# Optimization experiments

Hardware: AMD Instinct MI355X
Metric: run time of the kernel (lower is better)

Reference implementation:

```python
import jax, jax.numpy as jnp
import numpy as np

B, N, IN_DIM, HID = 8, 4096, 256, 256


def setup_inputs() -> dict:
    key = jax.random.key(0)
    ks = jax.random.split(key, 7)
    s_in = 1.0 / np.sqrt(IN_DIM)
    return {
        "x": jax.random.normal(ks[0], (B, N, IN_DIM), dtype=jnp.float32),
        "Wq": jax.random.uniform(ks[1], (IN_DIM, HID), jnp.float32, -s_in, s_in),
        "bq": jax.random.uniform(ks[2], (HID,), jnp.float32, -s_in, s_in),
        "Wk": jax.random.uniform(ks[3], (IN_DIM, HID), jnp.float32, -s_in, s_in),
        "bk": jax.random.uniform(ks[4], (HID,), jnp.float32, -s_in, s_in),
        "Wv": jax.random.uniform(ks[5], (IN_DIM, HID), jnp.float32, -s_in, s_in),
        "bv": jax.random.uniform(ks[6], (HID,), jnp.float32, -s_in, s_in),
    }


def reference(x, Wq, bq, Wk, bk, Wv, bv):
    # x: [B, N, in_dim]
    Q = jnp.einsum("bnd,dh->bnh", x, Wq) + bq  # [B, N, H]
    K = jnp.einsum("bnd,dh->bnh", x, Wk) + bk
    V = jnp.einsum("bnd,dh->bnh", x, Wv) + bv
    scale = 1.0 / jnp.sqrt(jnp.asarray(K.shape[-1], dtype=x.dtype))
    scores = jnp.einsum("bqh,bkh->bqk", Q, K) * scale  # [B, N, N]
    attn = jax.nn.softmax(scores, axis=-1)
    out = jnp.einsum("bqk,bkh->bqh", attn, V)  # [B, N, H]
    return out.mean(axis=1)  # [B, H]
```

## Files before the change

### kernel.cpp

```cpp
#include <hip/hip_runtime.h>
#include <hip/hip_bf16.h>


#define NTOK 4096
#define HDIM 256
#define NBATCH 8
#define SCALE 0.0625f

typedef __attribute__((ext_vector_type(8))) short short8_t;
typedef __attribute__((ext_vector_type(16))) float f32x16;

__device__ __forceinline__ unsigned short f2bf(float f) {
    unsigned u = __float_as_uint(f);
    u += 0x7fff + ((u >> 16) & 1);
    return (unsigned short)(u >> 16);
}

#define MFMA(a, b, c) __builtin_amdgcn_mfma_f32_32x32x16_bf16(a, b, c, 0, 0, 0)

__device__ __forceinline__ void async_cp16(const void* g, void* l) {
    __builtin_amdgcn_global_load_lds((const __attribute__((address_space(1))) void*)g,
                                     (__attribute__((address_space(3))) void*)l, 16, 0, 0);
}

__device__ __forceinline__ void stage_swz(unsigned short* lds, const unsigned short* src,
                                          int row0, int dbase, int w, int l) {
#pragma unroll
    for (int i = 0; i < 4; ++i) {
        int rloc = w * 32 + i * 8 + (l >> 3);
        int u = (l & 7) ^ (l >> 3);
        const unsigned short* g = src + (size_t)(row0 + rloc) * HDIM + dbase + u * 8;
        unsigned short* d = lds + (w * 32 + i * 8) * 64;
        async_cp16(g, d);
    }
}

__device__ __forceinline__ short8_t frd(const unsigned short* lds, int rb, int lo, int u) {
    return *(const short8_t*)(lds + ((rb * 32 + lo) * 8 + (u ^ (lo & 7))) * 8);
}

__global__ void zero_kernel(float* __restrict__ w, float* __restrict__ l, float* __restrict__ out) {
    int i = blockIdx.x * 256 + threadIdx.x;
    w[i] = 0.f;
    l[i] = 0.f;
    if (i < NBATCH * HDIM) out[i] = 0.f;
}

__global__ void convert_x(const float* __restrict__ x, unsigned short* __restrict__ xbf) {
    int i = (blockIdx.x * 256 + threadIdx.x) * 4;
    float4 v = *(const float4*)(x + i);
    ushort4 o;
    o.x = f2bf(v.x); o.y = f2bf(v.y); o.z = f2bf(v.z); o.w = f2bf(v.w);
    *(ushort4*)(xbf + i) = o;
}

__global__ void convert_wt(const float* __restrict__ Wq, const float* __restrict__ Wk,
                           const float* __restrict__ Wv, unsigned short* __restrict__ Wt) {
    int z = blockIdx.y;
    const float* W = (z == 0) ? Wq : (z == 1) ? Wk : Wv;
    unsigned short* o = Wt + z * 65536;
    int n = threadIdx.x;
    for (int kk = 0; kk < 32; ++kk) {
        int k = blockIdx.x * 32 + kk;
        o[n * 256 + k] = f2bf(W[k * 256 + n]);
    }
}

__global__ __launch_bounds__(256) void qkv_mfma(const unsigned short* __restrict__ xbf,
                                                const unsigned short* __restrict__ Wt,
                                                const float* __restrict__ bq, const float* __restrict__ bk,
                                                const float* __restrict__ bv,
                                                unsigned short* __restrict__ Qbf,
                                                unsigned short* __restrict__ Kbf,
                                                float* __restrict__ Vf) {
    const int z = blockIdx.z;
    const unsigned short* Wz = Wt + z * 65536;
    const float* bias = (z == 0) ? bq : (z == 1) ? bk : bv;
    const int m0 = blockIdx.x * 128, n0 = blockIdx.y * 128;
    const int t = threadIdx.x, w = t >> 6, l = t & 63, lo = l & 31, hi = l >> 5;
    const int rm = (w & 1) * 2, rn = (w >> 1) * 2;

    __shared__ __align__(16) char smem[32768];
    unsigned short* Xb = (unsigned short*)smem;
    unsigned short* Wb = (unsigned short*)(smem + 16384);

    f32x16 acc[2][2];
#pragma unroll
    for (int a = 0; a < 2; ++a)
#pragma unroll
        for (int c = 0; c < 2; ++c)
#pragma unroll
            for (int r = 0; r < 16; ++r) acc[a][c][r] = 0.f;

    for (int dc = 0; dc < 4; ++dc) {
        __syncthreads();
        stage_swz(Xb, xbf, m0, dc * 64, w, l);
        stage_swz(Wb, Wz, n0, dc * 64, w, l);
        __syncthreads();
#pragma unroll
        for (int ks = 0; ks < 4; ++ks) {
            int u = ks * 2 + hi;
            short8_t a0 = frd(Xb, rm + 0, lo, u);
            short8_t a1 = frd(Xb, rm + 1, lo, u);
            short8_t b0 = frd(Wb, rn + 0, lo, u);
            short8_t b1 = frd(Wb, rn + 1, lo, u);
            acc[0][0] = MFMA(a0, b0, acc[0][0]);
            acc[0][1] = MFMA(a0, b1, acc[0][1]);
            acc[1][0] = MFMA(a1, b0, acc[1][0]);
            acc[1][1] = MFMA(a1, b1, acc[1][1]);
        }
    }
    float bc0 = bias[n0 + (w >> 1) * 64 + lo];
    float bc1 = bias[n0 + (w >> 1) * 64 + 32 + lo];
#pragma unroll
    for (int mb = 0; mb < 2; ++mb)
#pragma unroll
        for (int r = 0; r < 16; ++r) {
            int row = m0 + (w & 1) * 64 + mb * 32 + (r & 3) + 8 * (r >> 2) + 4 * hi;
            int c0 = n0 + (w >> 1) * 64 + lo, c1 = c0 + 32;
            float v0 = acc[mb][0][r] + bc0;
            float v1 = acc[mb][1][r] + bc1;
            if (z == 2) {
                Vf[(size_t)row * HDIM + c0] = v0;
                Vf[(size_t)row * HDIM + c1] = v1;
            } else {
                unsigned short* o = (z == 0) ? Qbf : Kbf;
                o[(size_t)row * HDIM + c0] = f2bf(v0);
                o[(size_t)row * HDIM + c1] = f2bf(v1);
            }
        }
}

__global__ __launch_bounds__(256) void score_pass1(const unsigned short* __restrict__ Qbf,
                                                   const unsigned short* __restrict__ Kbf,
                                                   float* __restrict__ lsum) {
    const int b = blockIdx.z;
    const int q0 = blockIdx.x * 128;
    const int kslice = blockIdx.y;
    const int t = threadIdx.x, w = t >> 6, l = t & 63, lo = l & 31, hi = l >> 5;
    const int rq = (w & 1) * 2, rk = (w >> 1) * 2;
    const unsigned short* Qb = Qbf + (size_t)b * NTOK * HDIM;
    const unsigned short* Kb = Kbf + (size_t)b * NTOK * HDIM;

    __shared__ __align__(16) char smem[33792];
    unsigned short* Qs = (unsigned short*)smem;
    unsigned short* Ks = Qs + 8192;
    float* red = (float*)smem;

    float rs[2][16];
#pragma unroll
    for (int mb = 0; mb < 2; ++mb)
#pragma unroll
        for (int r = 0; r < 16; ++r) rs[mb][r] = 0.f;

    for (int kt = 0; kt < 4; ++kt) {
        const int k0 = kslice * 512 + kt * 128;
        f32x16 acc[2][2];
#pragma unroll
        for (int a = 0; a < 2; ++a)
#pragma unroll
            for (int c = 0; c < 2; ++c)
#pragma unroll
                for (int r = 0; r < 16; ++r) acc[a][c][r] = 0.f;

        for (int dc = 0; dc < 4; ++dc) {
            __syncthreads();
            stage_swz(Qs, Qb, q0, dc * 64, w, l);
            stage_swz(Ks, Kb, k0, dc * 64, w, l);
            __syncthreads();
#pragma unroll
            for (int ks = 0; ks < 4; ++ks) {
                int u = ks * 2 + hi;
                short8_t a0 = frd(Qs, rq + 0, lo, u);
                short8_t a1 = frd(Qs, rq + 1, lo, u);
                short8_t b0 = frd(Ks, rk + 0, lo, u);
                short8_t b1 = frd(Ks, rk + 1, lo, u);
                acc[0][0] = MFMA(a0, b0, acc[0][0]);
                acc[0][1] = MFMA(a0, b1, acc[0][1]);
                acc[1][0] = MFMA(a1, b0, acc[1][0]);
                acc[1][1] = MFMA(a1, b1, acc[1][1]);
            }
        }
#pragma unroll
        for (int mb = 0; mb < 2; ++mb)
#pragma unroll
            for (int r = 0; r < 16; ++r)
                rs[mb][r] += __expf(acc[mb][0][r] * SCALE) + __expf(acc[mb][1][r] * SCALE);
    }
    __syncthreads();
#pragma unroll
    for (int mb = 0; mb < 2; ++mb)
#pragma unroll
        for (int r = 0; r < 16; ++r) {
            int row = (w & 1) * 64 + mb * 32 + (r & 3) + 8 * (r >> 2) + 4 * hi;
            red[row * 66 + (w >> 1) * 32 + lo] = rs[mb][r];
        }
    __syncthreads();
    if (t < 128) {
        float s = 0.f;
#pragma unroll 8
        for (int j = 0; j < 64; ++j) s += red[t * 66 + j];
        atomicAdd(&lsum[b * NTOK + q0 + t], s);
    }
}

__global__ __launch_bounds__(256) void score_pass2(const unsigned short* __restrict__ Qbf,
                                                   const unsigned short* __restrict__ Kbf,
                                                   const float* __restrict__ lsum,
                                                   float* __restrict__ wsum) {
    const int b = blockIdx.z;
    const int k0 = blockIdx.x * 128;
    const int qslice = blockIdx.y;
    const int t = threadIdx.x, w = t >> 6, l = t & 63, lo = l & 31, hi = l >> 5;
    const int rq = (w & 1) * 2, rk = (w >> 1) * 2;
    const unsigned short* Qb = Qbf + (size_t)b * NTOK * HDIM;
    const unsigned short* Kb = Kbf + (size_t)b * NTOK * HDIM;

    __shared__ __align__(16) char smem[33792];
    __shared__ float linv_s[128];
    unsigned short* Qs = (unsigned short*)smem;
    unsigned short* Ks = Qs + 8192;
    float* red2 = (float*)smem;

    float cs0 = 0.f, cs1 = 0.f;

    for (int qt = 0; qt < 4; ++qt) {
        const int q0 = qslice * 512 + qt * 128;
        f32x16 acc[2][2];
#pragma unroll
        for (int a = 0; a < 2; ++a)
#pragma unroll
            for (int c = 0; c < 2; ++c)
#pragma unroll
                for (int r = 0; r < 16; ++r) acc[a][c][r] = 0.f;

        for (int dc = 0; dc < 4; ++dc) {
            __syncthreads();
            stage_swz(Qs, Qb, q0, dc * 64, w, l);
            stage_swz(Ks, Kb, k0, dc * 64, w, l);
            if (dc == 0 && t < 128) linv_s[t] = 1.0f / lsum[b * NTOK + q0 + t];
            __syncthreads();
#pragma unroll
            for (int ks = 0; ks < 4; ++ks) {
                int u = ks * 2 + hi;
                short8_t a0 = frd(Qs, rq + 0, lo, u);
                short8_t a1 = frd(Qs, rq + 1, lo, u);
                short8_t b0 = frd(Ks, rk + 0, lo, u);
                short8_t b1 = frd(Ks, rk + 1, lo, u);
                acc[0][0] = MFMA(a0, b0, acc[0][0]);
                acc[0][1] = MFMA(a0, b1, acc[0][1]);
                acc[1][0] = MFMA(a1, b0, acc[1][0]);
                acc[1][1] = MFMA(a1, b1, acc[1][1]);
            }
        }
#pragma unroll
        for (int mb = 0; mb < 2; ++mb)
#pragma unroll
            for (int r = 0; r < 16; ++r) {
                float li = linv_s[(w & 1) * 64 + mb * 32 + (r & 3) + 8 * (r >> 2) + 4 * hi];
                cs0 += __expf(acc[mb][0][r] * SCALE) * li;
                cs1 += __expf(acc[mb][1][r] * SCALE) * li;
            }
    }
    __syncthreads();
    red2[((w >> 1) * 64 + lo) * 5 + (w & 1) * 2 + hi] = cs0;
    red2[((w >> 1) * 64 + 32 + lo) * 5 + (w & 1) * 2 + hi] = cs1;
    __syncthreads();
    if (t < 128) {
        float s = red2[t * 5 + 0] + red2[t * 5 + 1] + red2[t * 5 + 2] + red2[t * 5 + 3];
        atomicAdd(&wsum[b * NTOK + k0 + t], s);
    }
}

__global__ __launch_bounds__(256) void finalize_kernel(const float* __restrict__ V,
                                                       const float* __restrict__ w,
                                                       float* __restrict__ out) {
    const int b = blockIdx.y;
    const int k0 = blockIdx.x * 256;
    const int h = threadIdx.x;
    __shared__ float wsh[256];
    wsh[h] = w[b * NTOK + k0 + h];
    __syncthreads();
    const float* Vb = V + ((size_t)b * NTOK + k0) * HDIM;
    float acc = 0.f;
#pragma unroll 4
    for (int kk = 0; kk < 256; ++kk) acc = fmaf(wsh[kk], Vb[(size_t)kk * HDIM + h], acc);
    atomicAdd(&out[b * HDIM + h], acc * (1.0f / (float)NTOK));
}

extern "C" void kernel_launch(void* const* d_in, const int* in_sizes, int n_in,
                              void* d_out, int out_size, void* d_ws, size_t ws_size,
                              hipStream_t stream) {
    const float* x  = (const float*)d_in[0];
    const float* Wq = (const float*)d_in[1];
    const float* bq = (const float*)d_in[2];
    const float* Wk = (const float*)d_in[3];
    const float* bk = (const float*)d_in[4];
    const float* Wv = (const float*)d_in[5];
    const float* bv = (const float*)d_in[6];
    float* out = (float*)d_out;

    const size_t BNH = (size_t)NBATCH * NTOK * HDIM;
    unsigned short* Wt  = (unsigned short*)d_ws;
    unsigned short* xbf = Wt + 3 * 65536;
    unsigned short* Qbf = xbf + BNH;
    unsigned short* Kbf = Qbf + BNH;
    float* Vf   = (float*)(Kbf + BNH);
    float* lsum = Vf + BNH;
    float* wsum = lsum + (size_t)NBATCH * NTOK;

    zero_kernel<<<dim3(128), dim3(256), 0, stream>>>(wsum, lsum, out);
    convert_x<<<dim3(8192), dim3(256), 0, stream>>>(x, xbf);
    convert_wt<<<dim3(8, 3), dim3(256), 0, stream>>>(Wq, Wk, Wv, Wt);
    qkv_mfma<<<dim3(256, 2, 3), dim3(256), 0, stream>>>(xbf, Wt, bq, bk, bv, Qbf, Kbf, Vf);
    score_pass1<<<dim3(32, 8, 8), dim3(256), 0, stream>>>(Qbf, Kbf, lsum);
    score_pass2<<<dim3(32, 8, 8), dim3(256), 0, stream>>>(Qbf, Kbf, lsum, wsum);
    finalize_kernel<<<dim3(16, 8), dim3(256), 0, stream>>>(Vf, wsum, out);
}
```

Before: 321.1 us.

## Keep Q/K rows in registers and double-buffer the streamed operand through LDS

Both score passes are restructured so each wave holds its 32 rows of the stationary operand (all 256 dims) in registers. The other operand is streamed in 64-row tiles through a double-buffered LDS ring with async global-to-LDS copies, which overlaps loads with MFMA work and halves the barriers per tile. The grid becomes 256 blocks of 512 threads with an XCD-aware mapping so a batch and slice stay on one XCD for L2 reuse. The cross-wave reduction is replaced by wave shuffles plus atomics. The costs are heavy register pressure from the 16 resident A fragments, fewer blocks in flight, and a per-tile global load of lsum in pass 2.

Result: faster. 279.1 us (-13.1%).

```diff
diff --git a/kernel.cpp b/kernel.cpp
--- a/kernel.cpp
+++ b/kernel.cpp
@@ -37,6 +37,25 @@
 
 __device__ __forceinline__ short8_t frd(const unsigned short* lds, int rb, int lo, int u) {
     return *(const short8_t*)(lds + ((rb * 32 + lo) * 8 + (u ^ (lo & 7))) * 8);
+}
+
+__device__ __forceinline__ void stage64(unsigned short* lds, const unsigned short* src,
+                                        int w, int l) {
+#pragma unroll
+    for (int j = 0; j < 4; ++j) {
+        int base = (w * 4 + j) * 64;
+        int idx = base + l;
+        int r = (idx >> 3) & 63;
+        int dc = idx >> 9;
+        int u = (idx & 7) ^ (r & 7);
+        const unsigned short* g = src + (size_t)r * HDIM + dc * 64 + u * 8;
+        async_cp16(g, lds + base * 8);
+    }
+}
+
+__device__ __forceinline__ short8_t krd(const unsigned short* lds, int r, int u) {
+    int dc = u >> 3, uu = u & 7;
+    return *(const short8_t*)(lds + ((dc * 64 + r) * 8 + (uu ^ (r & 7))) * 8);
 }
 
 __global__ void zero_kernel(float* __restrict__ w, float* __restrict__ l, float* __restrict__ out) {
@@ -131,144 +150,149 @@
         }
 }
 
-__global__ __launch_bounds__(256) void score_pass1(const unsigned short* __restrict__ Qbf,
-                                                   const unsigned short* __restrict__ Kbf,
-                                                   float* __restrict__ lsum) {
-    const int b = blockIdx.z;
-    const int q0 = blockIdx.x * 128;
-    const int kslice = blockIdx.y;
+__global__ __launch_bounds__(512, 2) void score_pass1(const unsigned short* __restrict__ Qbf,
+                                                      const unsigned short* __restrict__ Kbf,
+                                                      float* __restrict__ lsum) {
+    const int id = blockIdx.x;
+    const int xcd = id & 7, j = id >> 3;
+    const int qtile = j & 15, gh = j >> 4;
+    const int g = xcd * 2 + gh;
+    const int kslice = g & 1, b = g >> 1;
+
+    const int q0 = qtile * 256;
+    const int kbase = kslice * 2048;
     const int t = threadIdx.x, w = t >> 6, l = t & 63, lo = l & 31, hi = l >> 5;
-    const int rq = (w & 1) * 2, rk = (w >> 1) * 2;
     const unsigned short* Qb = Qbf + (size_t)b * NTOK * HDIM;
     const unsigned short* Kb = Kbf + (size_t)b * NTOK * HDIM;
 
-    __shared__ __align__(16) char smem[33792];
-    unsigned short* Qs = (unsigned short*)smem;
-    unsigned short* Ks = Qs + 8192;
-    float* red = (float*)smem;
-
-    float rs[2][16];
-#pragma unroll
-    for (int mb = 0; mb < 2; ++mb)
-#pragma unroll
-        for (int r = 0; r < 16; ++r) rs[mb][r] = 0.f;
-
-    for (int kt = 0; kt < 4; ++kt) {
-        const int k0 = kslice * 512 + kt * 128;
-        f32x16 acc[2][2];
-#pragma unroll
-        for (int a = 0; a < 2; ++a)
-#pragma unroll
-            for (int c = 0; c < 2; ++c)
-#pragma unroll
-                for (int r = 0; r < 16; ++r) acc[a][c][r] = 0.f;
-
-        for (int dc = 0; dc < 4; ++dc) {
-            __syncthreads();
-            stage_swz(Qs, Qb, q0, dc * 64, w, l);
-            stage_swz(Ks, Kb, k0, dc * 64, w, l);
-            __syncthreads();
-#pragma unroll
-            for (int ks = 0; ks < 4; ++ks) {
-                int u = ks * 2 + hi;
-                short8_t a0 = frd(Qs, rq + 0, lo, u);
-                short8_t a1 = frd(Qs, rq + 1, lo, u);
-                short8_t b0 = frd(Ks, rk + 0, lo, u);
-                short8_t b1 = frd(Ks, rk + 1, lo, u);
-                acc[0][0] = MFMA(a0, b0, acc[0][0]);
-                acc[0][1] = MFMA(a0, b1, acc[0][1]);
-                acc[1][0] = MFMA(a1, b0, acc[1][0]);
-                acc[1][1] = MFMA(a1, b1, acc[1][1]);
-            }
-        }
-#pragma unroll
-        for (int mb = 0; mb < 2; ++mb)
-#pragma unroll
-            for (int r = 0; r < 16; ++r)
-                rs[mb][r] += __expf(acc[mb][0][r] * SCALE) + __expf(acc[mb][1][r] * SCALE);
-    }
+    __shared__ __align__(16) unsigned short Kbuf[2][16384];
+
+    stage64(Kbuf[0], Kb + (size_t)kbase * HDIM, w, l);
+
+    short8_t A[16];
+    const unsigned short* qrow = Qb + (size_t)(q0 + w * 32 + lo) * HDIM + hi * 8;
+#pragma unroll
+    for (int st = 0; st < 16; ++st) A[st] = *(const short8_t*)(qrow + st * 16);
+
+    float rs[16];
+#pragma unroll
+    for (int r = 0; r < 16; ++r) rs[r] = 0.f;
+
     __syncthreads();
-#pragma unroll
-    for (int mb = 0; mb < 2; ++mb)
+
+    int cur = 0;
+    for (int kt = 0; kt < 32; ++kt) {
+        if (kt < 31) stage64(Kbuf[cur ^ 1], Kb + (size_t)(kbase + (kt + 1) * 64) * HDIM, w, l);
+        const unsigned short* KL = Kbuf[cur];
+        f32x16 acc0, acc1;
+#pragma unroll
+        for (int r = 0; r < 16; ++r) { acc0[r] = 0.f; acc1[r] = 0.f; }
+#pragma unroll
+        for (int st = 0; st < 16; ++st) {
+            int u = st * 2 + hi;
+            short8_t b0 = krd(KL, lo, u);
+            short8_t b1 = krd(KL, 32 + lo, u);
+            acc0 = MFMA(A[st], b0, acc0);
+            acc1 = MFMA(A[st], b1, acc1);
+        }
+#pragma unroll
+        for (int r = 0; r < 16; ++r)
+            rs[r] += __expf(acc0[r] * SCALE) + __expf(acc1[r] * SCALE);
+        __syncthreads();
+        cur ^= 1;
+    }
+
+#pragma unroll
+    for (int r = 0; r < 16; ++r) {
+        float v = rs[r];
+        v += __shfl_xor(v, 1);
+        v += __shfl_xor(v, 2);
+        v += __shfl_xor(v, 4);
+        v += __shfl_xor(v, 8);
+        v += __shfl_xor(v, 16);
+        rs[r] = v;
+    }
+    if (lo == 0) {
 #pragma unroll
         for (int r = 0; r < 16; ++r) {
-            int row = (w & 1) * 64 + mb * 32 + (r & 3) + 8 * (r >> 2) + 4 * hi;
-            red[row * 66 + (w >> 1) * 32 + lo] = rs[mb][r];
-        }
-    __syncthreads();
-    if (t < 128) {
-        float s = 0.f;
-#pragma unroll 8
-        for (int j = 0; j < 64; ++j) s += red[t * 66 + j];
-        atomicAdd(&lsum[b * NTOK + q0 + t], s);
-    }
-}
-
-__global__ __launch_bounds__(256) void score_pass2(const unsigned short* __restrict__ Qbf,
-                                                   const unsigned short* __restrict__ Kbf,
-                                                   const float* __restrict__ lsum,
-                                                   float* __restrict__ wsum) {
-    const int b = blockIdx.z;
-    const int k0 = blockIdx.x * 128;
-    const int qslice = blockIdx.y;
+            int row = q0 + w * 32 + (r & 3) + 8 * (r >> 2) + 4 * hi;
+            atomicAdd(&lsum[b * NTOK + row], rs[r]);
+        }
+    }
+}
+
+__global__ __launch_bounds__(512, 2) void score_pass2(const unsigned short* __restrict__ Qbf,
+                                                      const unsigned short* __restrict__ Kbf,
+                                                      const float* __restrict__ lsum,
+                                                      float* __restrict__ wsum) {
+    const int id = blockIdx.x;
+    const int xcd = id & 7, j = id >> 3;
+    const int ktile = j & 15, gh = j >> 4;
+    const int g = xcd * 2 + gh;
+    const int qslice = g & 1, b = g >> 1;
+
+    const int k0 = ktile * 256;
+    const int qbase = qslice * 2048;
     const int t = threadIdx.x, w = t >> 6, l = t & 63, lo = l & 31, hi = l >> 5;
-    const int rq = (w & 1) * 2, rk = (w >> 1) * 2;
     const unsigned short* Qb = Qbf + (size_t)b * NTOK * HDIM;
     const unsigned short* Kb = Kbf + (size_t)b * NTOK * HDIM;
-
-    __shared__ __align__(16) char smem[33792];
-    __shared__ float linv_s[128];
-    unsigned short* Qs = (unsigned short*)smem;
-    unsigned short* Ks = Qs + 8192;
-    float* red2 = (float*)smem;
-
-    float cs0 = 0.f, cs1 = 0.f;
-
-    for (int qt = 0; qt < 4; ++qt) {
-        const int q0 = qslice * 512 + qt * 128;
-        f32x16 acc[2][2];
-#pragma unroll
-        for (int a = 0; a < 2; ++a)
-#pragma unroll
-            for (int c = 0; c < 2; ++c)
-#pragma unroll
-                for (int r = 0; r < 16; ++r) acc[a][c][r] = 0.f;
-
-        for (int dc = 0; dc < 4; ++dc) {
-            __syncthreads();
-            stage_swz(Qs, Qb, q0, dc * 64, w, l);
-            stage_swz(Ks, Kb, k0, dc * 64, w, l);
-            if (dc == 0 && t < 128) linv_s[t] = 1.0f / lsum[b * NTOK + q0 + t];
-            __syncthreads();
-#pragma unroll
-            for (int ks = 0; ks < 4; ++ks) {
-                int u = ks * 2 + hi;
-                short8_t a0 = frd(Qs, rq + 0, lo, u);
-                short8_t a1 = frd(Qs, rq + 1, lo, u);
-                short8_t b0 = frd(Ks, rk + 0, lo, u);
-                short8_t b1 = frd(Ks, rk + 1, lo, u);
-                acc[0][0] = MFMA(a0, b0, acc[0][0]);
-                acc[0][1] = MFMA(a0, b1, acc[0][1]);
-                acc[1][0] = MFMA(a1, b0, acc[1][0]);
-                acc[1][1] = MFMA(a1, b1, acc[1][1]);
-            }
-        }
-#pragma unroll
-        for (int mb = 0; mb < 2; ++mb)
-#pragma unroll
-            for (int r = 0; r < 16; ++r) {
-                float li = linv_s[(w & 1) * 64 + mb * 32 + (r & 3) + 8 * (r >> 2) + 4 * hi];
-                cs0 += __expf(acc[mb][0][r] * SCALE) * li;
-                cs1 += __expf(acc[mb][1][r] * SCALE) * li;
-            }
-    }
+    const float* lb = lsum + (size_t)b * NTOK;
+
+    __shared__ __align__(16) unsigned short Qbuf[2][16384];
+
+    stage64(Qbuf[0], Qb + (size_t)qbase * HDIM, w, l);
+
+    short8_t A[16];
+    const unsigned short* krow = Kb + (size_t)(k0 + w * 32 + lo) * HDIM + hi * 8;
+#pragma unroll
+    for (int st = 0; st < 16; ++st) A[st] = *(const short8_t*)(krow + st * 16);
+
+    float cs[16];
+#pragma unroll
+    for (int r = 0; r < 16; ++r) cs[r] = 0.f;
+
     __syncthreads();
-    red2[((w >> 1) * 64 + lo) * 5 + (w & 1) * 2 + hi] = cs0;
-    red2[((w >> 1) * 64 + 32 + lo) * 5 + (w & 1) * 2 + hi] = cs1;
-    __syncthreads();
-    if (t < 128) {
-        float s = red2[t * 5 + 0] + red2[t * 5 + 1] + red2[t * 5 + 2] + red2[t * 5 + 3];
-        atomicAdd(&wsum[b * NTOK + k0 + t], s);
+
+    int cur = 0;
+    for (int qt = 0; qt < 32; ++qt) {
+        if (qt < 31) stage64(Qbuf[cur ^ 1], Qb + (size_t)(qbase + (qt + 1) * 64) * HDIM, w, l);
+        float linv0 = 1.0f / lb[qbase + qt * 64 + lo];
+        float linv1 = 1.0f / lb[qbase + qt * 64 + 32 + lo];
+        const unsigned short* QL = Qbuf[cur];
+        f32x16 acc0, acc1;
+#pragma unroll
+        for (int r = 0; r < 16; ++r) { acc0[r] = 0.f; acc1[r] = 0.f; }
+#pragma unroll
+        for (int st = 0; st < 16; ++st) {
+            int u = st * 2 + hi;
+            short8_t b0 = krd(QL, lo, u);
+            short8_t b1 = krd(QL, 32 + lo, u);
+            acc0 = MFMA(A[st], b0, acc0);
+            acc1 = MFMA(A[st], b1, acc1);
+        }
+#pragma unroll
+        for (int r = 0; r < 16; ++r)
+            cs[r] += __expf(acc0[r] * SCALE) * linv0 + __expf(acc1[r] * SCALE) * linv1;
+        __syncthreads();
+        cur ^= 1;
+    }
+
+#pragma unroll
+    for (int r = 0; r < 16; ++r) {
+        float v = cs[r];
+        v += __shfl_xor(v, 1);
+        v += __shfl_xor(v, 2);
+        v += __shfl_xor(v, 4);
+        v += __shfl_xor(v, 8);
+        v += __shfl_xor(v, 16);
+        cs[r] = v;
+    }
+    if (lo == 0) {
+#pragma unroll
+        for (int r = 0; r < 16; ++r) {
+            int row = k0 + w * 32 + (r & 3) + 8 * (r >> 2) + 4 * hi;
+            atomicAdd(&wsum[b * NTOK + row], cs[r]);
+        }
     }
 }
 
@@ -313,7 +337,7 @@
     convert_x<<<dim3(8192), dim3(256), 0, stream>>>(x, xbf);
     convert_wt<<<dim3(8, 3), dim3(256), 0, stream>>>(Wq, Wk, Wv, Wt);
     qkv_mfma<<<dim3(256, 2, 3), dim3(256), 0, stream>>>(xbf, Wt, bq, bk, bv, Qbf, Kbf, Vf);
-    score_pass1<<<dim3(32, 8, 8), dim3(256), 0, stream>>>(Qbf, Kbf, lsum);
-    score_pass2<<<dim3(32, 8, 8), dim3(256), 0, stream>>>(Qbf, Kbf, lsum, wsum);
+    score_pass1<<<dim3(256), dim3(512), 0, stream>>>(Qbf, Kbf, lsum);
+    score_pass2<<<dim3(256), dim3(512), 0, stream>>>(Qbf, Kbf, lsum, wsum);
     finalize_kernel<<<dim3(16, 8), dim3(256), 0, stream>>>(Vf, wsum, out);
 }
```
